# Optimization experiments

Measured on AMD Instinct MI355X. Metric: run time of the kernel, lower is better.

The kernel has to match this reference:

```python
import jax, jax.numpy as jnp
import numpy as np
from jax import lax

B, T, D, L, H = 512, 512, 64, 32, 128


def setup_inputs() -> dict:
    key = jax.random.key(0)
    ks = jax.random.split(key, 18)
    s = 0.08  # keep recurrent dynamics stable
    return {
        "x": jax.random.normal(ks[0], (B, T, D), dtype=jnp.float32),
        "eps": jax.random.normal(ks[1], (B, L), dtype=jnp.float32),
        "enc_W_ih": jax.random.normal(ks[2], (4 * H, D), dtype=jnp.float32) * s,
        "enc_W_hh": jax.random.normal(ks[3], (4 * H, H), dtype=jnp.float32) * s,
        "enc_b_ih": jax.random.normal(ks[4], (4 * H,), dtype=jnp.float32) * s,
        "enc_b_hh": jax.random.normal(ks[5], (4 * H,), dtype=jnp.float32) * s,
        "mu_W": jax.random.normal(ks[6], (L, H), dtype=jnp.float32) * s,
        "mu_b": jax.random.normal(ks[7], (L,), dtype=jnp.float32) * s,
        "lv_W": jax.random.normal(ks[8], (L, H), dtype=jnp.float32) * s,
        "lv_b": jax.random.normal(ks[9], (L,), dtype=jnp.float32) * s,
        "init_W": jax.random.normal(ks[10], (H, L), dtype=jnp.float32) * s,
        "init_b": jax.random.normal(ks[11], (H,), dtype=jnp.float32) * s,
        "dec_W_ih": jax.random.normal(ks[12], (4 * H, D), dtype=jnp.float32) * s,
        "dec_W_hh": jax.random.normal(ks[13], (4 * H, H), dtype=jnp.float32) * s,
        "dec_b_ih": jax.random.normal(ks[14], (4 * H,), dtype=jnp.float32) * s,
        "dec_b_hh": jax.random.normal(ks[15], (4 * H,), dtype=jnp.float32) * s,
        "out_W": jax.random.normal(ks[16], (D, H), dtype=jnp.float32) * s,
        "out_b": jax.random.normal(ks[17], (D,), dtype=jnp.float32) * s,
    }


def _lstm_update(gates, c):
    # PyTorch gate order: input, forget, cell(g), output
    i, f, g, o = jnp.split(gates, 4, axis=-1)
    c_new = jax.nn.sigmoid(f) * c + jax.nn.sigmoid(i) * jnp.tanh(g)
    h_new = jax.nn.sigmoid(o) * jnp.tanh(c_new)
    return h_new, c_new


def reference(x, eps, enc_W_ih, enc_W_hh, enc_b_ih, enc_b_hh,
              mu_W, mu_b, lv_W, lv_b, init_W, init_b,
              dec_W_ih, dec_W_hh, dec_b_ih, dec_b_hh, out_W, out_b):
    Bn, Tn, Dn = x.shape
    Hn = enc_W_hh.shape[1]

    # ---- encoder LSTM (batch_first) ----
    # precompute input projections for all timesteps: [T, B, 4H]
    gx = (jnp.einsum('btd,gd->btg', x, enc_W_ih) + enc_b_ih + enc_b_hh)
    gx = gx.transpose(1, 0, 2)

    def enc_step(carry, g):
        h, c = carry
        gates = g + h @ enc_W_hh.T
        h, c = _lstm_update(gates, c)
        return (h, c), None

    h0 = jnp.zeros((Bn, Hn), x.dtype)
    (hT, _), _ = lax.scan(enc_step, (h0, h0), gx)

    mu = hT @ mu_W.T + mu_b
    log_var = hT @ lv_W.T + lv_b
    z = mu + eps * jnp.exp(0.5 * log_var)  # reparameterize

    h_dec = z @ init_W.T + init_b  # decoder_hidden_init (no activation)
    c_dec = jnp.zeros_like(h_dec)
    inp0 = jnp.zeros((Bn, Dn), x.dtype)
    bd = dec_b_ih + dec_b_hh

    def dec_step(carry, _):
        h, c, inp = carry
        gates = inp @ dec_W_ih.T + h @ dec_W_hh.T + bd
        h, c = _lstm_update(gates, c)
        y = h @ out_W.T + out_b  # fc_decode_output; also next input
        return (h, c, y), y

    _, ys = lax.scan(dec_step, (h_dec, c_dec, inp0), None, length=Tn)
    x_rec = ys.transpose(1, 0, 2)  # [B, T, D]
    return x_rec, mu, log_var
```

## Files before the change

kernel.cpp:

```cpp
#include <hip/hip_runtime.h>

#define Bn 512
#define Tn 512
#define Dn 64
#define Hn 128
#define Ln 32
#define GXT 4128

typedef __attribute__((ext_vector_type(8))) short short8v;
typedef __attribute__((ext_vector_type(4))) float float4v;
typedef __attribute__((ext_vector_type(2))) float float2v;

__device__ __forceinline__ unsigned short f2bf(float f){
  unsigned int u = __float_as_uint(f);
  u += 0x7FFFu + ((u >> 16) & 1u);
  return (unsigned short)(u >> 16);
}

__device__ __forceinline__ short8v pack8(float4v a, float4v b){
  short8v r;
  r[0]=(short)f2bf(a[0]); r[1]=(short)f2bf(a[1]);
  r[2]=(short)f2bf(a[2]); r[3]=(short)f2bf(a[3]);
  r[4]=(short)f2bf(b[0]); r[5]=(short)f2bf(b[1]);
  r[6]=(short)f2bf(b[2]); r[7]=(short)f2bf(b[3]);
  return r;
}

__device__ __forceinline__ short8v load_wfrag(const float* __restrict__ W, int n, int k0, int ldk){
  const float* p = W + (size_t)n*(size_t)ldk + (size_t)k0;
  float4v a = *(const float4v*)p;
  float4v b = *(const float4v*)(p+4);
  return pack8(a,b);
}

__device__ __forceinline__ float4v mfma16(short8v a, short8v b, float4v c){
  return __builtin_amdgcn_mfma_f32_16x16x32_bf16(a, b, c, 0, 0, 0);
}

__device__ __forceinline__ float sigm(float v){
  return __builtin_amdgcn_rcpf(1.0f + __expf(-v));
}
__device__ __forceinline__ float tanh_(float v){
  return 1.0f - 2.0f*__builtin_amdgcn_rcpf(1.0f + __expf(2.0f*v));
}

__device__ __forceinline__ void bar_lds(){
  __builtin_amdgcn_sched_barrier(0);
  asm volatile("s_waitcnt lgkmcnt(0)" ::: "memory");
  __builtin_amdgcn_s_barrier();
  __builtin_amdgcn_sched_barrier(0);
}

__global__ __launch_bounds__(256) void weff_kernel(
    const float* __restrict__ dW_ih, const float* __restrict__ dW_hh,
    const float* __restrict__ db_ih, const float* __restrict__ db_hh,
    const float* __restrict__ oW,    const float* __restrict__ ob,
    float* __restrict__ ws)
{
  int id = blockIdx.x*256 + threadIdx.x;
  if (id < 512*128) {
    int n = id >> 7, h = id & 127;
    float s = dW_hh[id];
    #pragma unroll 8
    for (int d = 0; d < Dn; ++d) s += dW_ih[n*Dn + d] * oW[d*Hn + h];
    ws[id] = s;
  } else if (id < 512*128 + 512) {
    int n = id - 512*128;
    float s = db_ih[n] + db_hh[n];
    #pragma unroll 8
    for (int d = 0; d < Dn; ++d) s += dW_ih[n*Dn + d] * ob[d];
    ws[512*128 + n] = s;
  }
}

__global__ __launch_bounds__(512, 2) void vae_fused(
    const float* __restrict__ x,     const float* __restrict__ eps,
    const float* __restrict__ eW_ih, const float* __restrict__ eW_hh,
    const float* __restrict__ eb_ih, const float* __restrict__ eb_hh,
    const float* __restrict__ muW,   const float* __restrict__ mub,
    const float* __restrict__ lvW,   const float* __restrict__ lvb,
    const float* __restrict__ iW,    const float* __restrict__ ib,
    const float* __restrict__ dW_hh, const float* __restrict__ db_ih,
    const float* __restrict__ db_hh, const float* __restrict__ oW,
    const float* __restrict__ ob,    const float* __restrict__ ws,
    float* __restrict__ out)
{
  __shared__ __align__(16) char gxb[8*GXT];
  __shared__ __align__(16) unsigned short h_lds[2*2*128];
  __shared__ __align__(16) float sc_h[2*Hn];
  __shared__ __align__(16) float sc_mu[2*Ln];
  __shared__ __align__(16) float sc_lv[2*Ln];
  __shared__ __align__(16) float sc_z[2*Ln];

  const int tid  = threadIdx.x;
  const int lane = tid & 63;
  const int w    = tid >> 6;
  const int m    = lane & 15;
  const int q    = lane >> 4;
  const int hrow = m & 1;
  const int rsel = q & 1;
  const int jown = w*16 + m;
  const int b0   = blockIdx.x * 2;
  char* const hwq_p = (char*)h_lds + q*256 + ((2*jown) ^ (q<<4));
  const char* const hr_p = (const char*)h_lds + hrow*256 + ((q*16) ^ (hrow<<4));
  const char* const gx_p = gxb + jown*8;
  char* const gw_p = gxb + jown*8 + q*(2*GXT);

  if (tid < 256) ((int*)h_lds)[tid] = 0;

  short8v wih[8];
  short8v whh[16];
  #pragma unroll
  for (int nt = 0; nt < 4; ++nt) {
    #pragma unroll
    for (int kt = 0; kt < 2; ++kt) wih[nt*2+kt] = load_wfrag(eW_ih, nt*128 + jown, kt*32 + q*8, Dn);
    #pragma unroll
    for (int kt = 0; kt < 4; ++kt) whh[nt*4+kt] = load_wfrag(eW_hh, nt*128 + jown, kt*32 + q*8, Hn);
  }
  float bia[4];
  #pragma unroll
  for (int g = 0; g < 4; ++g) bia[g] = eb_ih[g*128 + jown] + eb_hh[g*128 + jown];

  const float* xbase = x + (size_t)(b0 + hrow)*Tn*Dn + (size_t)(m>>1)*Dn + q*8;
  float4v xc0,xc1,xc2,xc3, xn0,xn1,xn2,xn3;
  xc0 = *(const float4v*)(xbase+0);  xc1 = *(const float4v*)(xbase+4);
  xc2 = *(const float4v*)(xbase+32); xc3 = *(const float4v*)(xbase+36);

  float cst = 0.f, hval = 0.f;
  __syncthreads();

#define RH(RB,KB)  (*(const short8v*)(hr_p + (RB)*512 + (KB)))
#define RGX(S,NT)  (*(const float2v*)(gx_p + (S)*GXT + (NT)*1024))

#define BATCH(TB) do { \
    short8v xf0 = pack8(xc0, xc1); \
    short8v xf1 = pack8(xc2, xc3); \
    if ((TB) < 63) { \
      const float* xp = xbase + ((TB)+1)*512; \
      xn0 = *(const float4v*)(xp+0);  xn1 = *(const float4v*)(xp+4); \
      xn2 = *(const float4v*)(xp+32); xn3 = *(const float4v*)(xp+36); \
    } \
    float4v zz = {0.f,0.f,0.f,0.f}; \
    float4v c0_ = mfma16(xf0, wih[0], zz); \
    float4v c1_ = mfma16(xf0, wih[2], zz); \
    float4v c2_ = mfma16(xf0, wih[4], zz); \
    float4v c3_ = mfma16(xf0, wih[6], zz); \
    c0_ = mfma16(xf1, wih[1], c0_); \
    c1_ = mfma16(xf1, wih[3], c1_); \
    c2_ = mfma16(xf1, wih[5], c2_); \
    c3_ = mfma16(xf1, wih[7], c3_); \
    *(float2v*)(gw_p +       0) = (float2v){c0_[0]+bia[0], c0_[1]+bia[0]}; \
    *(float2v*)(gw_p +    1024) = (float2v){c1_[0]+bia[1], c1_[1]+bia[1]}; \
    *(float2v*)(gw_p +    2048) = (float2v){c2_[0]+bia[2], c2_[1]+bia[2]}; \
    *(float2v*)(gw_p +    3072) = (float2v){c3_[0]+bia[3], c3_[1]+bia[3]}; \
    *(float2v*)(gw_p + GXT +    0) = (float2v){c0_[2]+bia[0], c0_[3]+bia[0]}; \
    *(float2v*)(gw_p + GXT + 1024) = (float2v){c1_[2]+bia[1], c1_[3]+bia[1]}; \
    *(float2v*)(gw_p + GXT + 2048) = (float2v){c2_[2]+bia[2], c2_[3]+bia[2]}; \
    *(float2v*)(gw_p + GXT + 3072) = (float2v){c3_[2]+bia[3], c3_[3]+bia[3]}; \
    xc0=xn0; xc1=xn1; xc2=xn2; xc3=xn3; \
    bar_lds(); \
  } while(0)

#define NONLIN1(GI,GF,GG,GO, WB) do { \
    float c = sigm(GF)*cst + sigm(GI)*tanh_(GG); \
    cst = c; \
    hval = sigm(GO)*tanh_(c); \
    if (q < 2) *(unsigned short*)(hwq_p + (WB)*512) = f2bf(hval); \
  } while(0)

#define HH16(RB) \
    short8v hf0 = RH(RB,0), hf1 = RH(RB,64), hf2 = RH(RB,128), hf3 = RH(RB,192); \
    float4v zz = {0.f,0.f,0.f,0.f}; \
    float4v a0 = mfma16(hf0, whh[0],  zz); \
    float4v a1 = mfma16(hf0, whh[4],  zz); \
    float4v a2 = mfma16(hf0, whh[8],  zz); \
    float4v a3 = mfma16(hf0, whh[12], zz); \
    a0 = mfma16(hf1, whh[1],  a0); a1 = mfma16(hf1, whh[5],  a1); \
    a2 = mfma16(hf1, whh[9],  a2); a3 = mfma16(hf1, whh[13], a3); \
    a0 = mfma16(hf2, whh[2],  a0); a1 = mfma16(hf2, whh[6],  a1); \
    a2 = mfma16(hf2, whh[10], a2); a3 = mfma16(hf2, whh[14], a3); \
    a0 = mfma16(hf3, whh[3],  a0); a1 = mfma16(hf3, whh[7],  a1); \
    a2 = mfma16(hf3, whh[11], a2); a3 = mfma16(hf3, whh[15], a3);

#define ENC_STEP(S, RB) do { \
    float2v g0 = RGX(S,0), g1 = RGX(S,1), g2 = RGX(S,2), g3 = RGX(S,3); \
    HH16(RB); \
    float gi = rsel ? a0[1]+g0[1] : a0[0]+g0[0]; \
    float gf = rsel ? a1[1]+g1[1] : a1[0]+g1[0]; \
    float gg = rsel ? a2[1]+g2[1] : a2[0]+g2[0]; \
    float go = rsel ? a3[1]+g3[1] : a3[0]+g3[0]; \
    NONLIN1(gi, gf, gg, go, (RB)^1); \
    bar_lds(); \
  } while(0)

  #pragma unroll 1
  for (int tb = 0; tb < 64; ++tb) {
    BATCH(tb);
    ENC_STEP(0,0); ENC_STEP(1,1); ENC_STEP(2,0); ENC_STEP(3,1);
    ENC_STEP(4,0); ENC_STEP(5,1); ENC_STEP(6,0); ENC_STEP(7,1);
  }

  if (q < 2) sc_h[q*Hn + jown] = hval;
  __syncthreads();

  if (tid < 128) {
    const int isLv = tid >> 6;
    const int rr   = (tid >> 5) & 1;
    const int l    = tid & 31;
    const float* Wp = isLv ? lvW : muW;
    float s = isLv ? lvb[l] : mub[l];
    #pragma unroll
    for (int k = 0; k < Hn; k += 4) {
      float4v wv = *(const float4v*)(Wp + l*Hn + k);
      float4v hv = *(const float4v*)(sc_h + rr*Hn + k);
      s += wv[0]*hv[0] + wv[1]*hv[1] + wv[2]*hv[2] + wv[3]*hv[3];
    }
    out[(size_t)Bn*Tn*Dn + (size_t)isLv*Bn*Ln + (size_t)(b0+rr)*Ln + l] = s;
    (isLv ? sc_lv : sc_mu)[rr*Ln + l] = s;
  }
  __syncthreads();

  if (tid < 64) {
    int rr = tid >> 5, l = tid & 31;
    sc_z[rr*Ln+l] = sc_mu[rr*Ln+l] + eps[(size_t)(b0+rr)*Ln + l] * __expf(0.5f * sc_lv[rr*Ln+l]);
  }
  __syncthreads();

  if (tid < 256) {
    int rr = tid >> 7, jj = tid & 127;
    float s = ib[jj];
    #pragma unroll
    for (int l = 0; l < Ln; ++l) s += sc_z[rr*Ln + l] * iW[jj*Ln + l];
    *(unsigned short*)((char*)h_lds + rr*256 + ((2*jj) ^ (rr<<4))) = f2bf(s);
  }
  cst = 0.f;

  #pragma unroll
  for (int nt = 0; nt < 4; ++nt)
    #pragma unroll
    for (int kt = 0; kt < 4; ++kt) whh[nt*4+kt] = load_wfrag(dW_hh, nt*128 + jown, kt*32 + q*8, Hn);
  #pragma unroll
  for (int g = 0; g < 4; ++g) bia[g] = db_ih[g*128 + jown] + db_hh[g*128 + jown];
  const int ocol = (w & 3)*16 + m;
  short8v ow0 = load_wfrag(oW, ocol,  0 + q*8, Hn);
  short8v ow1 = load_wfrag(oW, ocol, 32 + q*8, Hn);
  short8v ow2 = load_wfrag(oW, ocol, 64 + q*8, Hn);
  short8v ow3 = load_wfrag(oW, ocol, 96 + q*8, Hn);
  const float obv = ob[ocol];
  __syncthreads();

  {
    HH16(0);
    float gi = (rsel ? a0[1] : a0[0]) + bia[0];
    float gf = (rsel ? a1[1] : a1[0]) + bia[1];
    float gg = (rsel ? a2[1] : a2[0]) + bia[2];
    float go = (rsel ? a3[1] : a3[0]) + bia[3];
    NONLIN1(gi, gf, gg, go, 1);
    bar_lds();
  }

  {
    const float* weff = ws;
    const float* beff = ws + 512*128;
    #pragma unroll
    for (int nt = 0; nt < 4; ++nt)
      #pragma unroll
      for (int kt = 0; kt < 4; ++kt) whh[nt*4+kt] = load_wfrag(weff, nt*128 + jown, kt*32 + q*8, Hn);
    #pragma unroll
    for (int g = 0; g < 4; ++g) bia[g] = beff[g*128 + jown];
  }

  float* outp0 = out + (size_t)(b0+0)*Tn*Dn;
  float* outp1 = out + (size_t)(b0+1)*Tn*Dn;

#define DEC_STEP(RB) do { \
    HH16(RB); \
    if (w < 4) { \
      float4v ya = mfma16(hf0, ow0, zz); \
      ya = mfma16(hf1, ow1, ya); ya = mfma16(hf2, ow2, ya); ya = mfma16(hf3, ow3, ya); \
      if (q == 0) { outp0[ocol] = ya[0] + obv; outp1[ocol] = ya[1] + obv; } \
    } \
    outp0 += Dn; outp1 += Dn; \
    float gi = (rsel ? a0[1] : a0[0]) + bia[0]; \
    float gf = (rsel ? a1[1] : a1[0]) + bia[1]; \
    float gg = (rsel ? a2[1] : a2[0]) + bia[2]; \
    float go = (rsel ? a3[1] : a3[0]) + bia[3]; \
    NONLIN1(gi, gf, gg, go, (RB)^1); \
    bar_lds(); \
  } while(0)

  #pragma unroll 1
  for (int i = 1; i < Tn-1; i += 2) {
    DEC_STEP(1);
    DEC_STEP(0);
  }
  DEC_STEP(1);

  if (w < 4) {
    short8v hf0 = RH(0,0), hf1 = RH(0,64), hf2 = RH(0,128), hf3 = RH(0,192);
    float4v ya = {0.f,0.f,0.f,0.f};
    ya = mfma16(hf0, ow0, ya); ya = mfma16(hf1, ow1, ya);
    ya = mfma16(hf2, ow2, ya); ya = mfma16(hf3, ow3, ya);
    if (q == 0) {
      outp0[ocol] = ya[0] + obv;
      outp1[ocol] = ya[1] + obv;
    }
  }
#undef DEC_STEP
#undef ENC_STEP
#undef HH16
#undef NONLIN1
#undef BATCH
#undef RGX
#undef RH
}

extern "C" void kernel_launch(void* const* d_in, const int* in_sizes, int n_in,
                              void* d_out, int out_size, void* d_ws, size_t ws_size,
                              hipStream_t stream) {
  (void)in_sizes; (void)n_in; (void)ws_size; (void)out_size;
  const float* x     = (const float*)d_in[0];
  const float* eps   = (const float*)d_in[1];
  const float* eW_ih = (const float*)d_in[2];
  const float* eW_hh = (const float*)d_in[3];
  const float* eb_ih = (const float*)d_in[4];
  const float* eb_hh = (const float*)d_in[5];
  const float* muW   = (const float*)d_in[6];
  const float* mub   = (const float*)d_in[7];
  const float* lvW   = (const float*)d_in[8];
  const float* lvb   = (const float*)d_in[9];
  const float* iW    = (const float*)d_in[10];
  const float* ib    = (const float*)d_in[11];
  const float* dW_ih = (const float*)d_in[12];
  const float* dW_hh = (const float*)d_in[13];
  const float* db_ih = (const float*)d_in[14];
  const float* db_hh = (const float*)d_in[15];
  const float* oW    = (const float*)d_in[16];
  const float* ob    = (const float*)d_in[17];
  float* out = (float*)d_out;
  float* ws  = (float*)d_ws;

  weff_kernel<<<dim3(258), dim3(256), 0, stream>>>(dW_ih, dW_hh, db_ih, db_hh, oW, ob, ws);
  vae_fused<<<dim3(256), dim3(512), 0, stream>>>(
      x, eps, eW_ih, eW_hh, eb_ih, eb_hh, muW, mub, lvW, lvb,
      iW, ib, dW_hh, db_ih, db_hh, oW, ob, ws, out);
}
```

Before: 581.3 us.

## Double-buffer encoder input projections and overlap them with recurrent steps

The encoder's input-projection batch (x·W_ih for 8 timesteps) now writes into one of two LDS buffers inside the first recurrent step of the current batch. This removes the separate barrier-bounded BATCH phase from the serial chain. The h and gx LDS layouts also change, dropping XOR swizzles in favour of padded row strides, and the gx reads shrink to scalar floats. In the decoder, the gate nonlinearity now comes before the output-projection MFMA so the recurrence critical path starts sooner. LDS usage roughly doubles for gx, which may pressure occupancy at two blocks per CU.

```diff
diff --git a/kernel.cpp b/kernel.cpp
--- a/kernel.cpp
+++ b/kernel.cpp
@@ -5,7 +5,10 @@
 #define Dn 64
 #define Hn 128
 #define Ln 32
-#define GXT 4128
+#define GXT   4112
+#define GXBUF (8*GXT)
+#define HRS   320
+#define HBUF  (2*HRS)
 
 typedef __attribute__((ext_vector_type(8))) short short8v;
 typedef __attribute__((ext_vector_type(4))) float float4v;
@@ -85,8 +88,8 @@
     const float* __restrict__ ob,    const float* __restrict__ ws,
     float* __restrict__ out)
 {
-  __shared__ __align__(16) char gxb[8*GXT];
-  __shared__ __align__(16) unsigned short h_lds[2*2*128];
+  __shared__ __align__(16) char gxb[2*GXBUF];
+  __shared__ __align__(16) char h_lds[2*HBUF];
   __shared__ __align__(16) float sc_h[2*Hn];
   __shared__ __align__(16) float sc_mu[2*Ln];
   __shared__ __align__(16) float sc_lv[2*Ln];
@@ -101,12 +104,12 @@
   const int rsel = q & 1;
   const int jown = w*16 + m;
   const int b0   = blockIdx.x * 2;
-  char* const hwq_p = (char*)h_lds + q*256 + ((2*jown) ^ (q<<4));
-  const char* const hr_p = (const char*)h_lds + hrow*256 + ((q*16) ^ (hrow<<4));
-  const char* const gx_p = gxb + jown*8;
-  char* const gw_p = gxb + jown*8 + q*(2*GXT);
-
-  if (tid < 256) ((int*)h_lds)[tid] = 0;
+  char* const hw_p  = h_lds + q*HRS + 2*jown;
+  const char* const hr_p = h_lds + hrow*HRS + q*16;
+  const char* const rgx_p = gxb + jown*8 + rsel*4;
+  char* const gwx_p = gxb + jown*8 + q*(2*GXT);
+
+  if (tid < (2*HBUF)/4) ((int*)h_lds)[tid] = 0;
 
   short8v wih[8];
   short8v whh[16];
@@ -121,25 +124,28 @@
   #pragma unroll
   for (int g = 0; g < 4; ++g) bia[g] = eb_ih[g*128 + jown] + eb_hh[g*128 + jown];
 
-  const float* xbase = x + (size_t)(b0 + hrow)*Tn*Dn + (size_t)(m>>1)*Dn + q*8;
+  const float* xptr = x + (size_t)(b0 + hrow)*Tn*Dn + (size_t)(m>>1)*Dn + q*8;
   float4v xc0,xc1,xc2,xc3, xn0,xn1,xn2,xn3;
-  xc0 = *(const float4v*)(xbase+0);  xc1 = *(const float4v*)(xbase+4);
-  xc2 = *(const float4v*)(xbase+32); xc3 = *(const float4v*)(xbase+36);
+  xc0 = *(const float4v*)(xptr+0);  xc1 = *(const float4v*)(xptr+4);
+  xc2 = *(const float4v*)(xptr+32); xc3 = *(const float4v*)(xptr+36);
+  xptr += 512;
+  int xnext = 1;
 
   float cst = 0.f, hval = 0.f;
   __syncthreads();
 
-#define RH(RB,KB)  (*(const short8v*)(hr_p + (RB)*512 + (KB)))
-#define RGX(S,NT)  (*(const float2v*)(gx_p + (S)*GXT + (NT)*1024))
-
-#define BATCH(TB) do { \
+#define RH(RB,KB)    (*(const short8v*)(hr_p + (RB)*HBUF + (KB)))
+#define RGX(CB,S,NT) (*(const float*)(rgx_p + (CB)*GXBUF + (S)*GXT + (NT)*1024))
+
+#define BATCH(PB) do { \
     short8v xf0 = pack8(xc0, xc1); \
     short8v xf1 = pack8(xc2, xc3); \
-    if ((TB) < 63) { \
-      const float* xp = xbase + ((TB)+1)*512; \
-      xn0 = *(const float4v*)(xp+0);  xn1 = *(const float4v*)(xp+4); \
-      xn2 = *(const float4v*)(xp+32); xn3 = *(const float4v*)(xp+36); \
+    if (xnext < 64) { \
+      xn0 = *(const float4v*)(xptr+0);  xn1 = *(const float4v*)(xptr+4); \
+      xn2 = *(const float4v*)(xptr+32); xn3 = *(const float4v*)(xptr+36); \
+      xptr += 512; \
     } \
+    ++xnext; \
     float4v zz = {0.f,0.f,0.f,0.f}; \
     float4v c0_ = mfma16(xf0, wih[0], zz); \
     float4v c1_ = mfma16(xf0, wih[2], zz); \
@@ -149,23 +155,23 @@
     c1_ = mfma16(xf1, wih[3], c1_); \
     c2_ = mfma16(xf1, wih[5], c2_); \
     c3_ = mfma16(xf1, wih[7], c3_); \
-    *(float2v*)(gw_p +       0) = (float2v){c0_[0]+bia[0], c0_[1]+bia[0]}; \
-    *(float2v*)(gw_p +    1024) = (float2v){c1_[0]+bia[1], c1_[1]+bia[1]}; \
-    *(float2v*)(gw_p +    2048) = (float2v){c2_[0]+bia[2], c2_[1]+bia[2]}; \
-    *(float2v*)(gw_p +    3072) = (float2v){c3_[0]+bia[3], c3_[1]+bia[3]}; \
-    *(float2v*)(gw_p + GXT +    0) = (float2v){c0_[2]+bia[0], c0_[3]+bia[0]}; \
-    *(float2v*)(gw_p + GXT + 1024) = (float2v){c1_[2]+bia[1], c1_[3]+bia[1]}; \
-    *(float2v*)(gw_p + GXT + 2048) = (float2v){c2_[2]+bia[2], c2_[3]+bia[2]}; \
-    *(float2v*)(gw_p + GXT + 3072) = (float2v){c3_[2]+bia[3], c3_[3]+bia[3]}; \
+    char* gp = gwx_p + (PB)*GXBUF; \
+    *(float2v*)(gp +       0) = (float2v){c0_[0]+bia[0], c0_[1]+bia[0]}; \
+    *(float2v*)(gp +    1024) = (float2v){c1_[0]+bia[1], c1_[1]+bia[1]}; \
+    *(float2v*)(gp +    2048) = (float2v){c2_[0]+bia[2], c2_[1]+bia[2]}; \
+    *(float2v*)(gp +    3072) = (float2v){c3_[0]+bia[3], c3_[1]+bia[3]}; \
+    *(float2v*)(gp + GXT +    0) = (float2v){c0_[2]+bia[0], c0_[3]+bia[0]}; \
+    *(float2v*)(gp + GXT + 1024) = (float2v){c1_[2]+bia[1], c1_[3]+bia[1]}; \
+    *(float2v*)(gp + GXT + 2048) = (float2v){c2_[2]+bia[2], c2_[3]+bia[2]}; \
+    *(float2v*)(gp + GXT + 3072) = (float2v){c3_[2]+bia[3], c3_[3]+bia[3]}; \
     xc0=xn0; xc1=xn1; xc2=xn2; xc3=xn3; \
-    bar_lds(); \
   } while(0)
 
 #define NONLIN1(GI,GF,GG,GO, WB) do { \
     float c = sigm(GF)*cst + sigm(GI)*tanh_(GG); \
     cst = c; \
     hval = sigm(GO)*tanh_(c); \
-    if (q < 2) *(unsigned short*)(hwq_p + (WB)*512) = f2bf(hval); \
+    if (q < 2) *(unsigned short*)(hw_p + (WB)*HBUF) = f2bf(hval); \
   } while(0)
 
 #define HH16(RB) \
@@ -182,25 +188,44 @@
     a0 = mfma16(hf3, whh[3],  a0); a1 = mfma16(hf3, whh[7],  a1); \
     a2 = mfma16(hf3, whh[11], a2); a3 = mfma16(hf3, whh[15], a3);
 
-#define ENC_STEP(S, RB) do { \
-    float2v g0 = RGX(S,0), g1 = RGX(S,1), g2 = RGX(S,2), g3 = RGX(S,3); \
-    HH16(RB); \
-    float gi = rsel ? a0[1]+g0[1] : a0[0]+g0[0]; \
-    float gf = rsel ? a1[1]+g1[1] : a1[0]+g1[0]; \
-    float gg = rsel ? a2[1]+g2[1] : a2[0]+g2[0]; \
-    float go = rsel ? a3[1]+g3[1] : a3[0]+g3[0]; \
-    NONLIN1(gi, gf, gg, go, (RB)^1); \
+#define ENC_STEP(S, CB) do { \
+    float g0 = RGX(CB,S,0), g1 = RGX(CB,S,1), g2 = RGX(CB,S,2), g3 = RGX(CB,S,3); \
+    HH16((S)&1); \
+    float gi = (rsel ? a0[1] : a0[0]) + g0; \
+    float gf = (rsel ? a1[1] : a1[0]) + g1; \
+    float gg = (rsel ? a2[1] : a2[0]) + g2; \
+    float go = (rsel ? a3[1] : a3[0]) + g3; \
+    NONLIN1(gi, gf, gg, go, ((S)&1)^1); \
     bar_lds(); \
   } while(0)
 
+#define ENC_STEP0(CB, PRODUCE) do { \
+    float g0 = RGX(CB,0,0), g1 = RGX(CB,0,1), g2 = RGX(CB,0,2), g3 = RGX(CB,0,3); \
+    HH16(0); \
+    float gi = (rsel ? a0[1] : a0[0]) + g0; \
+    float gf = (rsel ? a1[1] : a1[0]) + g1; \
+    float gg = (rsel ? a2[1] : a2[0]) + g2; \
+    float go = (rsel ? a3[1] : a3[0]) + g3; \
+    NONLIN1(gi, gf, gg, go, 1); \
+    if (PRODUCE) BATCH((CB)^1); \
+    bar_lds(); \
+  } while(0)
+
+#define ENC8(CB, PRODUCE) do { \
+    ENC_STEP0(CB, PRODUCE); \
+    ENC_STEP(1,CB); ENC_STEP(2,CB); ENC_STEP(3,CB); \
+    ENC_STEP(4,CB); ENC_STEP(5,CB); ENC_STEP(6,CB); ENC_STEP(7,CB); \
+  } while(0)
+
+  BATCH(0);
+  bar_lds();
   #pragma unroll 1
-  for (int tb = 0; tb < 64; ++tb) {
-    BATCH(tb);
-    ENC_STEP(0,0); ENC_STEP(1,1); ENC_STEP(2,0); ENC_STEP(3,1);
-    ENC_STEP(4,0); ENC_STEP(5,1); ENC_STEP(6,0); ENC_STEP(7,1);
-  }
-
-  if (q < 2) sc_h[q*Hn + jown] = hval;
+  for (int tb2 = 0; tb2 < 32; ++tb2) {
+    ENC8(0, 1);
+    ENC8(1, (tb2 < 31));
+  }
+
+  if (q < 2) sc_h[rsel*Hn + jown] = hval;
   __syncthreads();
 
   if (tid < 128) {
@@ -231,7 +256,7 @@
     float s = ib[jj];
     #pragma unroll
     for (int l = 0; l < Ln; ++l) s += sc_z[rr*Ln + l] * iW[jj*Ln + l];
-    *(unsigned short*)((char*)h_lds + rr*256 + ((2*jj) ^ (rr<<4))) = f2bf(s);
+    *(unsigned short*)(h_lds + rr*HRS + 2*jj) = f2bf(s);
   }
   cst = 0.f;
 
@@ -275,17 +300,17 @@
 
 #define DEC_STEP(RB) do { \
     HH16(RB); \
+    float gi = (rsel ? a0[1] : a0[0]) + bia[0]; \
+    float gf = (rsel ? a1[1] : a1[0]) + bia[1]; \
+    float gg = (rsel ? a2[1] : a2[0]) + bia[2]; \
+    float go = (rsel ? a3[1] : a3[0]) + bia[3]; \
+    NONLIN1(gi, gf, gg, go, (RB)^1); \
     if (w < 4) { \
       float4v ya = mfma16(hf0, ow0, zz); \
       ya = mfma16(hf1, ow1, ya); ya = mfma16(hf2, ow2, ya); ya = mfma16(hf3, ow3, ya); \
       if (q == 0) { outp0[ocol] = ya[0] + obv; outp1[ocol] = ya[1] + obv; } \
     } \
     outp0 += Dn; outp1 += Dn; \
-    float gi = (rsel ? a0[1] : a0[0]) + bia[0]; \
-    float gf = (rsel ? a1[1] : a1[0]) + bia[1]; \
-    float gg = (rsel ? a2[1] : a2[0]) + bia[2]; \
-    float go = (rsel ? a3[1] : a3[0]) + bia[3]; \
-    NONLIN1(gi, gf, gg, go, (RB)^1); \
     bar_lds(); \
   } while(0)
 
@@ -307,6 +332,8 @@
     }
   }
 #undef DEC_STEP
+#undef ENC8
+#undef ENC_STEP0
 #undef ENC_STEP
 #undef HH16
 #undef NONLIN1
```

Measured after the change: 510.3 us. -12.2%, faster.
